# Performance work log

Measured on AMD Instinct MI355X. Metric: run time of the kernel, lower is better.

## Reference

```python
import jax, jax.numpy as jnp
import numpy as np

B, S, D = 2, 2048, 1024
H, DK, DV = 16, 64, 64


def setup_inputs() -> dict:
    key = jax.random.key(0)
    ks = jax.random.split(key, 9)
    s = 0.02
    return {
        "x": jax.random.normal(ks[0], (B, S, D), dtype=jnp.float32),
        "mask": jnp.zeros((B, S), dtype=bool),  # True = padded position
        "Wq": jax.random.normal(ks[1], (D, H * DK), dtype=jnp.float32) * s,
        "bq": jnp.zeros((H * DK,), dtype=jnp.float32),
        "Wk": jax.random.normal(ks[2], (D, H * DK), dtype=jnp.float32) * s,
        "bk": jnp.zeros((H * DK,), dtype=jnp.float32),
        "Wv": jax.random.normal(ks[3], (D, H * DV), dtype=jnp.float32) * s,
        "bv": jnp.zeros((H * DV,), dtype=jnp.float32),
        "Wo": jax.random.normal(ks[4], (H * DV, D), dtype=jnp.float32) * s,
        "bo": jnp.zeros((D,), dtype=jnp.float32),
    }


def reference(x, mask, Wq, bq, Wk, bk, Wv, bv, Wo, bo):
    Bx, Sx, _ = x.shape
    # projections -> [B, H, S, dk/dv]
    q = (x @ Wq + bq).reshape(Bx, Sx, H, DK).transpose(0, 2, 1, 3)
    k = (x @ Wk + bk).reshape(Bx, Sx, H, DK).transpose(0, 2, 1, 3)
    v = (x @ Wv + bv).reshape(Bx, Sx, H, DV).transpose(0, 2, 1, 3)
    # scaled QK^T: [B, H, Sq, Sk]
    scores = jnp.einsum("bhqd,bhkd->bhqk", q, k) / jnp.sqrt(jnp.float32(DK))
    neg_inf = jnp.float32(-jnp.inf)
    # padding mask: True masks out key positions
    scores = jnp.where(mask[:, None, None, :], neg_inf, scores)
    # causal mask
    causal = jnp.triu(jnp.ones((Sx, Sx), dtype=bool), k=1)
    scores = jnp.where(causal[None, None, :, :], neg_inf, scores)
    attn = jax.nn.softmax(scores, axis=-1)
    out = jnp.einsum("bhqk,bhkd->bhqd", attn, v)  # [B, H, S, dv]
    out = out.transpose(0, 2, 1, 3).reshape(Bx, Sx, H * DV)
    return out @ Wo + bo
```

## Files before the change

### kernel.cpp

```cpp
#include <hip/hip_runtime.h>
#include <stdint.h>

typedef __bf16 bf16_t;
typedef __bf16 bf16x8 __attribute__((ext_vector_type(8)));
typedef float f32x4 __attribute__((ext_vector_type(4)));

#define S_LEN 2048
#define D_MODEL 1024
#define NH 16
#define DKV 64
#define BATCH 2

#define QSCALE 0.1803368801111204f

__device__ __forceinline__ uint16_t f2bfu(float f) {
    union { float f; uint32_t u; } c; c.f = f;
    return (uint16_t)((c.u + 0x7fffu + ((c.u >> 16) & 1u)) >> 16);
}
__device__ __forceinline__ bf16_t f2bf(float f) {
    union { uint16_t s; bf16_t b; } o; o.s = f2bfu(f);
    return o.b;
}
__device__ __forceinline__ uint32_t pack2t(float lo, float hi) {
    union { float f; uint32_t u; } a, b; a.f = lo; b.f = hi;
    return __builtin_amdgcn_perm(b.u, a.u, 0x07060302);
}
__device__ __forceinline__ uint32_t pack2r(float lo, float hi) {
    union { float f; uint32_t u; } a, b; a.f = lo; b.f = hi;
    uint32_t alo = a.u + 0x7fffu + ((a.u >> 16) & 1u);
    uint32_t bhi = b.u + 0x7fffu + ((b.u >> 16) & 1u);
    return __builtin_amdgcn_perm(bhi, alo, 0x07060302);
}
__device__ __forceinline__ float exp2_native(float x) {
    float r;
    asm("v_exp_f32 %0, %1" : "=v"(r) : "v"(x));
    return r;
}
__device__ __forceinline__ void gld_lds16(const bf16_t* g, bf16_t* l) {
    __builtin_amdgcn_global_load_lds(
        (const __attribute__((address_space(1))) void*)g,
        (__attribute__((address_space(3))) void*)l, 16, 0, 0);
}

__global__ __launch_bounds__(256) void k_prep(
    const float* __restrict__ x, bf16_t* __restrict__ xb,
    const float* __restrict__ Wq, const float* __restrict__ Wk,
    const float* __restrict__ Wv, const float* __restrict__ Wo,
    bf16_t* __restrict__ WqkvT, bf16_t* __restrict__ WoT) {
    __shared__ float tile[64][65];
    int bid = blockIdx.x;
    if (bid < 4096) {
        int i = (bid * 256 + threadIdx.x) * 4;
        float4 v = *(const float4*)(x + i);
        xb[i + 0] = f2bf(v.x);
        xb[i + 1] = f2bf(v.y);
        xb[i + 2] = f2bf(v.z);
        xb[i + 3] = f2bf(v.w);
        return;
    }
    int b2 = bid - 4096;
    int k0 = (b2 & 15) * 64;
    int n0 = (b2 >> 4) * 64;
    const float* W; bf16_t* WT; int np, nw;
    if (n0 < 3072) {
        W = (n0 < 1024) ? Wq : (n0 < 2048) ? Wk : Wv;
        np = n0 & 1023; WT = WqkvT; nw = n0;
    } else {
        W = Wo; np = n0 - 3072; WT = WoT; nw = n0 - 3072;
    }
    int tx = threadIdx.x & 63, ty = threadIdx.x >> 6;
    #pragma unroll
    for (int r = ty; r < 64; r += 4)
        tile[r][tx] = W[(size_t)(k0 + r) * 1024 + np + tx];
    __syncthreads();
    #pragma unroll
    for (int r = ty; r < 64; r += 4)
        WT[(size_t)(nw + r) * 1024 + k0 + tx] = f2bf(tile[tx][r]);
}

#define BM 128
#define BN 128

__global__ __launch_bounds__(256) void k_gemm_qkv(
    const bf16_t* __restrict__ A, const bf16_t* __restrict__ BT, int K,
    const float* __restrict__ bias0, const float* __restrict__ bias1,
    const float* __restrict__ bias2,
    bf16_t* __restrict__ outQ, bf16_t* __restrict__ outK, bf16_t* __restrict__ outVt) {
    __shared__ __align__(16) bf16_t smem[4 * 128 * 32];
    bf16_t* const As0 = smem;
    bf16_t* const As1 = smem + 128 * 32;
    bf16_t* const Bs0 = smem + 2 * 128 * 32;
    bf16_t* const Bs1 = smem + 3 * 128 * 32;
    int m0 = blockIdx.x * BM;
    int n0 = blockIdx.y * BN;
    int t = threadIdx.x;
    int wid = t >> 6, lane = t & 63, l15 = lane & 15, quad = lane >> 4;
    int wr = (wid >> 1) * 64, wc = (wid & 1) * 64;
    int sr = t >> 2;
    int sc = (t & 3) ^ ((sr >> 1) & 3);
    int sl = (t & 3) * 8;
    const f32x4 fzero = {0.f, 0.f, 0.f, 0.f};
    f32x4 acc[4][4];
    #pragma unroll
    for (int i = 0; i < 4; i++)
        #pragma unroll
        for (int j = 0; j < 4; j++) acc[i][j] = fzero;

    int secb = n0 >> 10;
    int colA = (quad ^ ((l15 >> 1) & 3)) << 3;

    auto STAGE = [&](bf16_t* __restrict__ Ad, bf16_t* __restrict__ Bd, int k0) {
        #pragma unroll
        for (int p = 0; p < 2; p++) {
            int r = p * 64 + sr;
            gld_lds16(&A[(size_t)(m0 + r) * K + k0 + sc * 8], &Ad[r * 32 + sl]);
            gld_lds16(&BT[(size_t)(n0 + r) * K + k0 + sc * 8], &Bd[r * 32 + sl]);
        }
    };

    auto STEP = [&](const bf16_t* __restrict__ Ar, const bf16_t* __restrict__ Br,
                    bf16_t* __restrict__ Aw, bf16_t* __restrict__ Bw, int i) {
        if (i + 1 < 32) STAGE(Aw, Bw, (i + 1) * 32);
        bf16x8 af[4], bfr[4];
        #pragma unroll
        for (int mt = 0; mt < 4; mt++)
            af[mt] = *(const bf16x8*)&Ar[(wr + mt * 16 + l15) * 32 + colA];
        #pragma unroll
        for (int nt = 0; nt < 4; nt++)
            bfr[nt] = *(const bf16x8*)&Br[(wc + nt * 16 + l15) * 32 + colA];
        __builtin_amdgcn_s_setprio(1);
        if (secb == 2) {
            #pragma unroll
            for (int mt = 0; mt < 4; mt++)
                #pragma unroll
                for (int nt = 0; nt < 4; nt++)
                    acc[mt][nt] = __builtin_amdgcn_mfma_f32_16x16x32_bf16(
                        af[mt], bfr[nt], acc[mt][nt], 0, 0, 0);
        } else {
            #pragma unroll
            for (int i2 = 0; i2 < 4; i2++)
                #pragma unroll
                for (int j = 0; j < 4; j++)
                    acc[i2][j] = __builtin_amdgcn_mfma_f32_16x16x32_bf16(
                        bfr[i2], af[j], acc[i2][j], 0, 0, 0);
        }
        __builtin_amdgcn_s_setprio(0);
        if (i + 1 < 32) __syncthreads();
    };

    STAGE(As0, Bs0, 0);
    __syncthreads();
    for (int i = 0; i < 32; i += 2) {
        STEP(As0, Bs0, As1, Bs1, i);
        STEP(As1, Bs1, As0, Bs0, i + 1);
    }

    if (secb == 2) {
        __syncthreads();
        bf16_t* const Ct = smem;
        int nbase = n0 & 1023;
        #pragma unroll
        for (int mt = 0; mt < 4; mt++) {
            #pragma unroll
            for (int nt = 0; nt < 4; nt++) {
                int dl = wc + nt * 16 + l15;
                float bv = bias2[nbase + dl];
                int sl2 = wr + mt * 16 + quad * 4;
                uint2 pk;
                pk.x = pack2t(acc[mt][nt][0] + bv, acc[mt][nt][1] + bv);
                pk.y = pack2t(acc[mt][nt][2] + bv, acc[mt][nt][3] + bv);
                int c4 = (sl2 >> 2) ^ ((dl & 7) << 1);
                *(uint2*)&Ct[dl * 128 + c4 * 4] = pk;
            }
        }
        __syncthreads();
        int b = m0 >> 11, sb = m0 & 2047;
        #pragma unroll
        for (int rr = 0; rr < 8; rr++) {
            int row = rr * 16 + (t >> 4);
            int s8 = t & 15;
            int c4 = (s8 * 2) ^ ((row & 7) << 1);
            uint4 vv = *(const uint4*)&Ct[row * 128 + c4 * 4];
            int nn = nbase + row;
            int h = nn >> 6, d = nn & 63;
            *(uint4*)&outVt[(((size_t)(b * NH + h)) * DKV + d) * S_LEN + sb + s8 * 8] = vv;
        }
        return;
    }

    {
        const float* bias = (secb == 0) ? bias0 : bias1;
        bf16_t* outP = (secb == 0) ? outQ : outK;
        float scale = (secb == 0) ? QSCALE : 1.0f;
        #pragma unroll
        for (int i = 0; i < 4; i++) {
            #pragma unroll
            for (int j = 0; j < 4; j++) {
                int nn = (n0 + wc + i * 16 + quad * 4) & 1023;
                float4 bv = *(const float4*)&bias[nn];
                int gr = m0 + wr + j * 16 + l15;
                int b = gr >> 11, s = gr & 2047;
                int h = nn >> 6, d0 = nn & 63;
                float v0 = (acc[i][j][0] + bv.x) * scale;
                float v1 = (acc[i][j][1] + bv.y) * scale;
                float v2 = (acc[i][j][2] + bv.z) * scale;
                float v3 = (acc[i][j][3] + bv.w) * scale;
                uint2 pk;
                pk.x = pack2r(v0, v1);
                pk.y = pack2r(v2, v3);
                *(uint2*)&outP[(((size_t)(b * NH + h)) * S_LEN + s) * DKV + d0] = pk;
            }
        }
    }
}

__global__ __launch_bounds__(256) void k_gemm_out(
    const bf16_t* __restrict__ A, const bf16_t* __restrict__ BT, int N, int K,
    const float* __restrict__ bias, float* __restrict__ outF) {
    __shared__ __align__(16) bf16_t As[128 * 64];
    __shared__ __align__(16) bf16_t Bs[64 * 64];
    int m0 = blockIdx.x * 128;
    int n0 = blockIdx.y * 64;
    int t = threadIdx.x;
    int wid = t >> 6, lane = t & 63, l15 = lane & 15, quad = lane >> 4;
    int wr = wid * 32;
    int srow = t >> 3;
    int schunk = (t & 7) ^ (srow & 7);
    int sldst = (t & 7) * 8;
    const f32x4 fzero = {0.f, 0.f, 0.f, 0.f};
    f32x4 acc[4][2];
    #pragma unroll
    for (int i = 0; i < 4; i++)
        #pragma unroll
        for (int j = 0; j < 2; j++) acc[i][j] = fzero;

    int r7 = l15 & 7;
    for (int k0 = 0; k0 < K; k0 += 64) {
        #pragma unroll
        for (int p = 0; p < 4; p++) {
            int r = p * 32 + srow;
            gld_lds16(&A[(size_t)(m0 + r) * K + k0 + schunk * 8], &As[r * 64 + sldst]);
        }
        #pragma unroll
        for (int p = 0; p < 2; p++) {
            int r = p * 32 + srow;
            gld_lds16(&BT[(size_t)(n0 + r) * K + k0 + schunk * 8], &Bs[r * 64 + sldst]);
        }
        __syncthreads();
        #pragma unroll
        for (int kk = 0; kk < 64; kk += 32) {
            int g = quad + (kk >> 3);
            int col = ((g ^ r7) << 3);
            bf16x8 af[2], bfr[4];
            #pragma unroll
            for (int j = 0; j < 2; j++)
                af[j] = *(const bf16x8*)&As[(wr + j * 16 + l15) * 64 + col];
            #pragma unroll
            for (int i = 0; i < 4; i++)
                bfr[i] = *(const bf16x8*)&Bs[(i * 16 + l15) * 64 + col];
            #pragma unroll
            for (int i = 0; i < 4; i++)
                #pragma unroll
                for (int j = 0; j < 2; j++)
                    acc[i][j] = __builtin_amdgcn_mfma_f32_16x16x32_bf16(
                        bfr[i], af[j], acc[i][j], 0, 0, 0);
        }
        __syncthreads();
    }

    #pragma unroll
    for (int i = 0; i < 4; i++) {
        #pragma unroll
        for (int j = 0; j < 2; j++) {
            int nc = n0 + i * 16 + quad * 4;
            float4 bv = *(const float4*)&bias[nc];
            int mr = m0 + wr + j * 16 + l15;
            float4 o;
            o.x = acc[i][j][0] + bv.x;
            o.y = acc[i][j][1] + bv.y;
            o.z = acc[i][j][2] + bv.z;
            o.w = acc[i][j][3] + bv.w;
            *(float4*)&outF[(size_t)mr * N + nc] = o;
        }
    }
}

__global__ __launch_bounds__(256, 4) void k_attn11(
    const bf16_t* __restrict__ Q, const bf16_t* __restrict__ Kg,
    const bf16_t* __restrict__ Vt, const unsigned char* __restrict__ mask,
    bf16_t* __restrict__ O) {
    __shared__ __align__(16) bf16_t Ks0[64 * 64];
    __shared__ __align__(16) bf16_t Ks1[64 * 64];
    __shared__ __align__(16) bf16_t Vs0[64 * 64];
    __shared__ __align__(16) bf16_t Vs1[64 * 64];
    __shared__ __align__(16) bf16_t Ps[64 * 64];

    int bid = blockIdx.x;
    int bh = bid & 31;
    int u = bid >> 5;
    int a = u & 7, g2 = u >> 3;
    int qt = (g2 == 0) ? 31 - a : (g2 == 1) ? a : (g2 == 2) ? 23 - a : 8 + a;
    int b = bh >> 4, h = bh & 15;
    int t = threadIdx.x;
    int w = t >> 6, lane = t & 63, l15 = lane & 15, quad = lane >> 4;
    int r7 = l15 & 7;

    bool maskany;
    {
        const uint2* mrow = (const uint2*)&mask[b * S_LEN];
        uint2 m0 = mrow[lane], m1 = mrow[lane + 64];
        uint2 m2 = mrow[lane + 128], m3 = mrow[lane + 192];
        uint32_t mo = (m0.x | m0.y) | (m1.x | m1.y) | (m2.x | m2.y) | (m3.x | m3.y);
        maskany = __any(mo != 0);
    }

    const bf16_t* Qrow = Q + ((size_t)bh * S_LEN + qt * 64 + w * 16 + l15) * DKV;
    bf16x8 qf0 = *(const bf16x8*)&Qrow[quad * 8];
    bf16x8 qf1 = *(const bf16x8*)&Qrow[32 + quad * 8];

    const bf16_t* Kbh = Kg + (size_t)bh * S_LEN * DKV;
    const bf16_t* Vbh = Vt + (size_t)bh * DKV * S_LEN;

    const f32x4 fzero = {0.f, 0.f, 0.f, 0.f};
    f32x4 oacc[4];
    f32x4 lacc = fzero;
    #pragma unroll
    for (int nt = 0; nt < 4; nt++) oacc[nt] = fzero;

    const bf16_t one_b = (bf16_t)1.0f;
    const bf16x8 onesf = {one_b, one_b, one_b, one_b, one_b, one_b, one_b, one_b};

    int qg = qt * 64 + w * 16 + l15;
    int qmin = qt * 64 + w * 16;

    int sr = t >> 3;
    int sc = (t & 7) ^ (sr & 7);
    int sl = (t & 7) * 8;

    #pragma unroll
    for (int p = 0; p < 2; p++) {
        int r = p * 32 + sr;
        gld_lds16(&Kbh[(size_t)r * DKV + sc * 8], &Ks0[r * 64 + sl]);
        gld_lds16(&Vbh[(size_t)r * S_LEN + sc * 8], &Vs0[r * 64 + sl]);
    }
    __syncthreads();

    auto TILE = [&](const bf16_t* __restrict__ Kr, const bf16_t* __restrict__ Vr,
                    bf16_t* __restrict__ Kw, bf16_t* __restrict__ Vw, int kt) {
        if (kt < qt) {
            int kb2 = (kt + 1) * 64;
            #pragma unroll
            for (int p = 0; p < 2; p++) {
                int r = p * 32 + sr;
                gld_lds16(&Kbh[(size_t)(kb2 + r) * DKV + sc * 8], &Kw[r * 64 + sl]);
                gld_lds16(&Vbh[(size_t)r * S_LEN + kb2 + sc * 8], &Vw[r * 64 + sl]);
            }
        }
        int kbase = kt * 64;

        f32x4 sacc[4];
        #pragma unroll
        for (int mt = 0; mt < 4; mt++) sacc[mt] = fzero;
        #pragma unroll
        for (int kk = 0; kk < 64; kk += 32) {
            bf16x8 qf = kk ? qf1 : qf0;
            int col = (((quad + (kk >> 3)) ^ r7) << 3);
            bf16x8 af[4];
            #pragma unroll
            for (int mt = 0; mt < 4; mt++)
                af[mt] = *(const bf16x8*)&Kr[(mt * 16 + l15) * 64 + col];
            __builtin_amdgcn_s_setprio(1);
            #pragma unroll
            for (int mt = 0; mt < 4; mt++)
                sacc[mt] = __builtin_amdgcn_mfma_f32_16x16x32_bf16(af[mt], qf, sacc[mt], 0, 0, 0);
            __builtin_amdgcn_s_setprio(0);
        }

        if (maskany) {
            #pragma unroll
            for (int mt = 0; mt < 4; mt++) {
                uint32_t mb = *(const uint32_t*)&mask[b * S_LEN + kbase + mt * 16 + quad * 4];
                #pragma unroll
                for (int r = 0; r < 4; r++)
                    sacc[mt][r] += (float)((mb >> (8 * r)) & 0xffu) * -1e30f;
            }
        }
        if (kt == qt) {
            #pragma unroll
            for (int mt = 0; mt < 4; mt++) {
                int kgb = kbase + mt * 16 + quad * 4;
                #pragma unroll
                for (int r = 0; r < 4; r++)
                    if (kgb + r > qg) sacc[mt][r] = -1e30f;
            }
        }
        #pragma unroll
        for (int mt = 0; mt < 4; mt++) {
            uint2 pk;
            pk.x = pack2t(exp2_native(sacc[mt][0]), exp2_native(sacc[mt][1]));
            pk.y = pack2t(exp2_native(sacc[mt][2]), exp2_native(sacc[mt][3]));
            int pc = (mt * 2 + (quad >> 1)) ^ r7;
            *(uint2*)&Ps[(w * 16 + l15) * 64 + pc * 8 + (quad & 1) * 4] = pk;
        }

        #pragma unroll
        for (int kk = 0; kk < 64; kk += 32) {
            int vcol = (((quad + (kk >> 3)) ^ r7) << 3);
            bf16x8 pf = *(const bf16x8*)&Ps[(w * 16 + l15) * 64 + vcol];
            bf16x8 vf[4];
            #pragma unroll
            for (int nt = 0; nt < 4; nt++)
                vf[nt] = *(const bf16x8*)&Vr[(nt * 16 + l15) * 64 + vcol];
            __builtin_amdgcn_s_setprio(1);
            #pragma unroll
            for (int nt = 0; nt < 4; nt++)
                oacc[nt] = __builtin_amdgcn_mfma_f32_16x16x32_bf16(pf, vf[nt], oacc[nt], 0, 0, 0);
            lacc = __builtin_amdgcn_mfma_f32_16x16x32_bf16(pf, onesf, lacc, 0, 0, 0);
            __builtin_amdgcn_s_setprio(0);
        }

        if (kt < qt) __syncthreads();
    };

    for (int kt = 0; kt <= qt; kt += 2) {
        TILE(Ks0, Vs0, Ks1, Vs1, kt);
        if (kt + 1 <= qt) TILE(Ks1, Vs1, Ks0, Vs0, kt + 1);
    }

    #pragma unroll
    for (int r = 0; r < 4; r++) {
        float l = lacc[r];
        float invl = l > 0.f ? 1.f / l : 0.f;
        int q = qt * 64 + w * 16 + quad * 4 + r;
        #pragma unroll
        for (int nt = 0; nt < 4; nt++) {
            int d = nt * 16 + l15;
            O[((size_t)b * S_LEN + q) * D_MODEL + h * DKV + d] = f2bf(oacc[nt][r] * invl);
        }
    }
}

extern "C" void kernel_launch(void* const* d_in, const int* in_sizes, int n_in,
                              void* d_out, int out_size, void* d_ws, size_t ws_size,
                              hipStream_t stream) {
    const float* x = (const float*)d_in[0];
    const unsigned char* mask = (const unsigned char*)d_in[1];
    const float* Wq = (const float*)d_in[2];
    const float* bq = (const float*)d_in[3];
    const float* Wk = (const float*)d_in[4];
    const float* bk = (const float*)d_in[5];
    const float* Wv = (const float*)d_in[6];
    const float* bv = (const float*)d_in[7];
    const float* Wo = (const float*)d_in[8];
    const float* bo = (const float*)d_in[9];
    float* out = (float*)d_out;

    char* ws = (char*)d_ws;
    const size_t MB = 1024 * 1024;
    bf16_t* xb    = (bf16_t*)(ws + 0 * MB);
    bf16_t* WqkvT = (bf16_t*)(ws + 8 * MB);
    bf16_t* WoT   = (bf16_t*)(ws + 14 * MB);
    bf16_t* Qb    = (bf16_t*)(ws + 16 * MB);
    bf16_t* Kb    = (bf16_t*)(ws + 24 * MB);
    bf16_t* Vtb   = (bf16_t*)(ws + 32 * MB);
    bf16_t* AOb   = (bf16_t*)(ws + 40 * MB);

    k_prep<<<dim3(4096 + 1024), dim3(256), 0, stream>>>(
        x, xb, Wq, Wk, Wv, Wo, WqkvT, WoT);
    k_gemm_qkv<<<dim3(32, 24), dim3(256), 0, stream>>>(
        xb, WqkvT, 1024, bq, bk, bv, Qb, Kb, Vtb);
    k_attn11<<<dim3(1024), dim3(256), 0, stream>>>(Qb, Kb, Vtb, mask, AOb);
    k_gemm_out<<<dim3(32, 16), dim3(256), 0, stream>>>(
        AOb, WoT, 1024, 1024, bo, out);
}
```

Baseline: 176.5 us.

## Double-buffer LDS in output projection GEMM with K-step of 32

```diff
diff --git a/kernel.cpp b/kernel.cpp
--- a/kernel.cpp
+++ b/kernel.cpp
@@ -217,16 +217,18 @@
 __global__ __launch_bounds__(256) void k_gemm_out(
     const bf16_t* __restrict__ A, const bf16_t* __restrict__ BT, int N, int K,
     const float* __restrict__ bias, float* __restrict__ outF) {
-    __shared__ __align__(16) bf16_t As[128 * 64];
-    __shared__ __align__(16) bf16_t Bs[64 * 64];
+    __shared__ __align__(16) bf16_t As0[128 * 32];
+    __shared__ __align__(16) bf16_t As1[128 * 32];
+    __shared__ __align__(16) bf16_t Bs0[64 * 32];
+    __shared__ __align__(16) bf16_t Bs1[64 * 32];
     int m0 = blockIdx.x * 128;
     int n0 = blockIdx.y * 64;
     int t = threadIdx.x;
     int wid = t >> 6, lane = t & 63, l15 = lane & 15, quad = lane >> 4;
     int wr = wid * 32;
-    int srow = t >> 3;
-    int schunk = (t & 7) ^ (srow & 7);
-    int sldst = (t & 7) * 8;
+    int sr = t >> 2;
+    int sc = (t & 3) ^ ((sr >> 1) & 3);
+    int sl = (t & 3) * 8;
     const f32x4 fzero = {0.f, 0.f, 0.f, 0.f};
     f32x4 acc[4][2];
     #pragma unroll
@@ -234,38 +236,43 @@
         #pragma unroll
         for (int j = 0; j < 2; j++) acc[i][j] = fzero;
 
-    int r7 = l15 & 7;
-    for (int k0 = 0; k0 < K; k0 += 64) {
-        #pragma unroll
-        for (int p = 0; p < 4; p++) {
-            int r = p * 32 + srow;
-            gld_lds16(&A[(size_t)(m0 + r) * K + k0 + schunk * 8], &As[r * 64 + sldst]);
-        }
+    int colA = (quad ^ ((l15 >> 1) & 3)) << 3;
+
+    auto STAGE = [&](bf16_t* __restrict__ Ad, bf16_t* __restrict__ Bd, int k0) {
         #pragma unroll
         for (int p = 0; p < 2; p++) {
-            int r = p * 32 + srow;
-            gld_lds16(&BT[(size_t)(n0 + r) * K + k0 + schunk * 8], &Bs[r * 64 + sldst]);
-        }
-        __syncthreads();
-        #pragma unroll
-        for (int kk = 0; kk < 64; kk += 32) {
-            int g = quad + (kk >> 3);
-            int col = ((g ^ r7) << 3);
-            bf16x8 af[2], bfr[4];
+            int r = p * 64 + sr;
+            gld_lds16(&A[(size_t)(m0 + r) * K + k0 + sc * 8], &Ad[r * 32 + sl]);
+        }
+        gld_lds16(&BT[(size_t)(n0 + sr) * K + k0 + sc * 8], &Bd[sr * 32 + sl]);
+    };
+
+    auto STEP = [&](const bf16_t* __restrict__ Ar, const bf16_t* __restrict__ Br,
+                    bf16_t* __restrict__ Aw, bf16_t* __restrict__ Bw, int i) {
+        if (i + 1 < 32) STAGE(Aw, Bw, (i + 1) * 32);
+        bf16x8 af[2], bfr[4];
+        #pragma unroll
+        for (int j = 0; j < 2; j++)
+            af[j] = *(const bf16x8*)&Ar[(wr + j * 16 + l15) * 32 + colA];
+        #pragma unroll
+        for (int i2 = 0; i2 < 4; i2++)
+            bfr[i2] = *(const bf16x8*)&Br[(i2 * 16 + l15) * 32 + colA];
+        __builtin_amdgcn_s_setprio(1);
+        #pragma unroll
+        for (int i2 = 0; i2 < 4; i2++)
             #pragma unroll
             for (int j = 0; j < 2; j++)
-                af[j] = *(const bf16x8*)&As[(wr + j * 16 + l15) * 64 + col];
-            #pragma unroll
-            for (int i = 0; i < 4; i++)
-                bfr[i] = *(const bf16x8*)&Bs[(i * 16 + l15) * 64 + col];
-            #pragma unroll
-            for (int i = 0; i < 4; i++)
-                #pragma unroll
-                for (int j = 0; j < 2; j++)
-                    acc[i][j] = __builtin_amdgcn_mfma_f32_16x16x32_bf16(
-                        bfr[i], af[j], acc[i][j], 0, 0, 0);
-        }
-        __syncthreads();
+                acc[i2][j] = __builtin_amdgcn_mfma_f32_16x16x32_bf16(
+                    bfr[i2], af[j], acc[i2][j], 0, 0, 0);
+        __builtin_amdgcn_s_setprio(0);
+        if (i + 1 < 32) __syncthreads();
+    };
+
+    STAGE(As0, Bs0, 0);
+    __syncthreads();
+    for (int i = 0; i < 32; i += 2) {
+        STEP(As0, Bs0, As1, Bs1, i);
+        STEP(As1, Bs1, As0, Bs0, i + 1);
     }
 
     #pragma unroll
```

After: 174.6 us (median of 2 runs). No clear change (-1.1%).
